# Performance work log

Hardware: AMD Instinct MI355X
Metric: run time of the kernel (lower is better)

The kernel has to match this reference:

```python
import jax, jax.numpy as jnp
import numpy as np

N, E, D = 50000, 640000, 128

def setup_inputs() -> dict:
    key = jax.random.key(0)
    ks = jax.random.split(key, 7)
    feat = jax.random.normal(ks[0], (N, D), dtype=jnp.float32)
    node_alpha = jax.random.uniform(ks[1], (N, 1), dtype=jnp.float32)
    edge_src = jax.random.randint(ks[2], (E,), 0, N, dtype=jnp.int32)
    edge_dst = jax.random.randint(ks[3], (E,), 0, N, dtype=jnp.int32)
    edge_e = jax.random.uniform(ks[4], (E,), dtype=jnp.float32)
    # xavier_normal with relu gain for a square D x D linear
    gain = float(np.sqrt(2.0))
    std = gain * float(np.sqrt(2.0 / (D + D)))
    W = jax.random.normal(ks[5], (D, D), dtype=jnp.float32) * std
    b = jnp.zeros((D,), dtype=jnp.float32)
    return {"feat": feat, "node_alpha": node_alpha, "edge_src": edge_src,
            "edge_dst": edge_dst, "edge_e": edge_e, "W": W, "b": b}

def reference(feat, node_alpha, edge_src, edge_dst, edge_e, W, b):
    # dropout prob = 0 -> identity
    feat_dst = node_alpha[:, 0:1] * feat  # residual term, n_dst == N
    # per-edge: e * Linear(z_src)   (Linear: z @ W.T + b)
    z_src = feat[edge_src]                              # [E, D] gather
    msg = edge_e[:, None] * (z_src @ W.T + b)           # [E, D]
    # mean over each dst node's mailbox
    summed = jax.ops.segment_sum(msg, edge_dst, num_segments=N)          # [N, D]
    deg = jax.ops.segment_sum(jnp.ones((E,), jnp.float32), edge_dst, num_segments=N)
    mean = summed / jnp.maximum(deg, 1.0)[:, None]
    f = jax.nn.relu(mean)
    return f + feat_dst
```

## Files before the change

kernel.cpp:

```cpp
#include <hip/hip_runtime.h>

#define D 128
#define CAP 48
#define NB 196
#define BCAP 3712
#define SPB 5
#define POISON_INT ((int)0xAAAAAAAA)


typedef __attribute__((ext_vector_type(8))) short short8;
typedef __attribute__((ext_vector_type(4))) float f32x4;

__device__ __forceinline__ float bf16bits_to_f(unsigned int u16) {
    return __uint_as_float(u16 << 16);
}
__device__ __forceinline__ unsigned int f_to_bf16bits(float f) {
    return (__float_as_uint(f) + 0x8000u) >> 16;
}
__device__ __forceinline__ void bf16_split(float x, unsigned int& hb, unsigned int& lb) {
    unsigned int u = __float_as_uint(x);
    hb = (u + 0x8000u) >> 16;
    float r = x - __uint_as_float(hb << 16);
    lb = (__float_as_uint(r) + 0x8000u) >> 16;
}

__global__ __launch_bounds__(512) void combo_k(
    const float* __restrict__ feat,
    const float* __restrict__ W,
    const float* __restrict__ b,
    const int* __restrict__ esrc,
    const int* __restrict__ edst,
    const float* __restrict__ ee,
    int* __restrict__ bktcur,
    uint2* __restrict__ bkt,
    unsigned short* __restrict__ h,
    int N, int E, int GB, int n_strips)
{
    __shared__ unsigned int Ab[2][16 * 128];
    __shared__ int hist[256];
    __shared__ int hbase[256];

    const int tid = threadIdx.x;

    if ((int)blockIdx.x >= GB) {
        const int e0 = ((int)blockIdx.x - GB) * 2048 + tid;
        for (int i = tid; i < 256; i += 512) hist[i] = 0;
        __syncthreads();

        int dd[4]; unsigned int pk[4]; int ofs[4]; bool vv[4];
#pragma unroll
        for (int k = 0; k < 4; ++k) {
            int idx = e0 + k * 512;
            vv[k] = idx < E;
            int s = vv[k] ? idx : 0;
            dd[k] = edst[s];
            pk[k] = (f_to_bf16bits(ee[s]) << 16) | ((unsigned int)esrc[s] & 0xFFFFu);
            ofs[k] = vv[k] ? atomicAdd(&hist[dd[k] >> 8], 1) : 0;
        }
        __syncthreads();
        for (int i = tid; i < NB; i += 512) {
            int c = hist[i];
            hbase[i] = c ? (atomicAdd(&bktcur[i], c) - POISON_INT) : 0;
        }
        __syncthreads();
#pragma unroll
        for (int k = 0; k < 4; ++k) {
            if (vv[k]) {
                int bn = dd[k] >> 8;
                int pos = hbase[bn] + ofs[k];
                if (pos < BCAP)
                    bkt[(size_t)bn * BCAP + pos] =
                        make_uint2(pk[k], (unsigned int)(dd[k] & 255));
            }
        }
        return;
    }

    const int w  = tid >> 6;
    const int l  = tid & 63;
    const int lr = l & 15;
    const int cg = l >> 4;

    const int col = w * 16 + lr;
    short8 bh[4], bl[4];
    {
        const float* wrow = W + (size_t)col * D + cg * 8;
#pragma unroll
        for (int kc = 0; kc < 4; ++kc) {
            float4 w0 = *(const float4*)&wrow[kc * 32];
            float4 w1 = *(const float4*)&wrow[kc * 32 + 4];
            unsigned int hb[8], lb[8];
            bf16_split(w0.x, hb[0], lb[0]); bf16_split(w0.y, hb[1], lb[1]);
            bf16_split(w0.z, hb[2], lb[2]); bf16_split(w0.w, hb[3], lb[3]);
            bf16_split(w1.x, hb[4], lb[4]); bf16_split(w1.y, hb[5], lb[5]);
            bf16_split(w1.z, hb[6], lb[6]); bf16_split(w1.w, hb[7], lb[7]);
            union { unsigned int u[4]; short8 s; } uh, ul;
#pragma unroll
            for (int t2 = 0; t2 < 4; ++t2) {
                uh.u[t2] = hb[2 * t2] | (hb[2 * t2 + 1] << 16);
                ul.u[t2] = lb[2 * t2] | (lb[2 * t2 + 1] << 16);
            }
            bh[kc] = uh.s; bl[kc] = ul.s;
        }
    }
    const float bcol = b[col];

    const int sr  = tid >> 5;
    const int sc  = tid & 31;
    const int scs = sc ^ (sr & 7);

    const int strip0 = (int)blockIdx.x * SPB;

    {
        int row = strip0 * 16 + sr;
        float4 a = make_float4(0.f, 0.f, 0.f, 0.f);
        if (row < N) a = *(const float4*)&feat[(size_t)row * D + sc * 4];
        unsigned int hb2, lb2; uint4 pv;
        bf16_split(a.x, hb2, lb2); pv.x = (hb2 << 16) | lb2;
        bf16_split(a.y, hb2, lb2); pv.y = (hb2 << 16) | lb2;
        bf16_split(a.z, hb2, lb2); pv.z = (hb2 << 16) | lb2;
        bf16_split(a.w, hb2, lb2); pv.w = (hb2 << 16) | lb2;
        *(uint4*)&Ab[0][sr * 128 + scs * 4] = pv;
    }
    __syncthreads();

    for (int s = 0; s < SPB; ++s) {
        int sg = strip0 + s;
        if (sg >= n_strips) break;

        float4 anext = make_float4(0.f, 0.f, 0.f, 0.f);
        bool more = (s + 1 < SPB) && (sg + 1 < n_strips);
        if (more) {
            int row = (sg + 1) * 16 + sr;
            if (row < N) anext = *(const float4*)&feat[(size_t)row * D + sc * 4];
        }

        const unsigned int* Ar = &Ab[s & 1][0];
        f32x4 ahh = {0.f, 0.f, 0.f, 0.f};
        f32x4 ahl = {0.f, 0.f, 0.f, 0.f};
        f32x4 alh = {0.f, 0.f, 0.f, 0.f};
#pragma unroll
        for (int kc = 0; kc < 4; ++kc) {
            int ch0 = kc * 8 + cg * 2;
            uint4 ua = *(const uint4*)&Ar[lr * 128 + (((ch0    ) ^ (lr & 7)) << 2)];
            uint4 ub = *(const uint4*)&Ar[lr * 128 + (((ch0 + 1) ^ (lr & 7)) << 2)];
            union { unsigned int u[4]; short8 s; } ah, al;
            ah.u[0] = (ua.x >> 16) | (ua.y & 0xFFFF0000u);
            ah.u[1] = (ua.z >> 16) | (ua.w & 0xFFFF0000u);
            ah.u[2] = (ub.x >> 16) | (ub.y & 0xFFFF0000u);
            ah.u[3] = (ub.z >> 16) | (ub.w & 0xFFFF0000u);
            al.u[0] = (ua.x & 0xFFFFu) | (ua.y << 16);
            al.u[1] = (ua.z & 0xFFFFu) | (ua.w << 16);
            al.u[2] = (ub.x & 0xFFFFu) | (ub.y << 16);
            al.u[3] = (ub.z & 0xFFFFu) | (ub.w << 16);
            ahh = __builtin_amdgcn_mfma_f32_16x16x32_bf16(ah.s, bh[kc], ahh, 0, 0, 0);
            ahl = __builtin_amdgcn_mfma_f32_16x16x32_bf16(ah.s, bl[kc], ahl, 0, 0, 0);
            alh = __builtin_amdgcn_mfma_f32_16x16x32_bf16(al.s, bh[kc], alh, 0, 0, 0);
        }

        {
            int rbase = sg * 16 + cg * 4;
#pragma unroll
            for (int q = 0; q < 4; ++q) {
                int row = rbase + q;
                if (row < N) {
                    float v = ahh[q] + ahl[q] + alh[q] + bcol;
                    h[(size_t)row * D + col] = (unsigned short)f_to_bf16bits(v);
                }
            }
        }

        if (more) {
            unsigned int hb2, lb2; uint4 pv;
            bf16_split(anext.x, hb2, lb2); pv.x = (hb2 << 16) | lb2;
            bf16_split(anext.y, hb2, lb2); pv.y = (hb2 << 16) | lb2;
            bf16_split(anext.z, hb2, lb2); pv.z = (hb2 << 16) | lb2;
            bf16_split(anext.w, hb2, lb2); pv.w = (hb2 << 16) | lb2;
            *(uint4*)&Ab[(s + 1) & 1][sr * 128 + scs * 4] = pv;
        }
        __syncthreads();
    }
}

#define ACC_EDGE(e_, hv_) do { \
    a0 += (e_) * bf16bits_to_f((hv_).x & 0xFFFFu); \
    a1 += (e_) * bf16bits_to_f((hv_).x >> 16); \
    a2 += (e_) * bf16bits_to_f((hv_).y & 0xFFFFu); \
    a3 += (e_) * bf16bits_to_f((hv_).y >> 16); \
} while (0)

__global__ __launch_bounds__(512) void agg_bin_k(
    const float* __restrict__ feat,
    const unsigned short* __restrict__ h,
    const uint2* __restrict__ bkt,
    const int* __restrict__ bktcur,
    const float* __restrict__ alpha,
    float* __restrict__ out,
    int N)
{
    __shared__ int cnt[32];
    __shared__ __align__(16) unsigned int list[32 * CAP];

    const int tid  = threadIdx.x;
    const int bin  = (int)blockIdx.x >> 3;
    const int oct  = (int)blockIdx.x & 7;
    const int node0 = bin * 256 + oct * 32;

    if (tid < 32) cnt[tid] = 0;
    __syncthreads();

    int m = bktcur[bin] - POISON_INT;
    if (m > BCAP) m = BCAP;
    const uint2* B = bkt + (size_t)bin * BCAP;

    uint2 ebuf[8]; bool ev[8];
#pragma unroll
    for (int r = 0; r < 8; ++r) {
        int idx = tid + r * 512;
        ev[r] = idx < m;
        ebuf[r] = B[ev[r] ? idx : 0];
    }
#pragma unroll
    for (int r = 0; r < 8; ++r) {
        int ld = ev[r] ? ((int)ebuf[r].y - oct * 32) : -1;
        if (ld >= 0 && ld < 32) {
            int s = atomicAdd(&cnt[ld], 1);
            if (s < CAP) list[ld * CAP + s] = ebuf[r].x;
        }
    }
    __syncthreads();

    const int l32 = tid & 31;
    const int nl0 = (tid >> 5) * 2;

    for (int nl = nl0; nl < nl0 + 2; ++nl) {
        int node = node0 + nl;
        if (node >= N) break;
        int deg = cnt[nl];
        int c = deg > CAP ? CAP : deg;
        const unsigned int* L = &list[nl * CAP];

        float a0 = 0.f, a1 = 0.f, a2 = 0.f, a3 = 0.f;
        int j = 0;
        for (; j + 8 <= c; j += 8) {
            uint4 qa = *(const uint4*)&L[j];
            uint4 qb = *(const uint4*)&L[j + 4];
            uint2 hv0 = ((const uint2*)(h + (size_t)(qa.x & 0xFFFFu) * D))[l32];
            uint2 hv1 = ((const uint2*)(h + (size_t)(qa.y & 0xFFFFu) * D))[l32];
            uint2 hv2 = ((const uint2*)(h + (size_t)(qa.z & 0xFFFFu) * D))[l32];
            uint2 hv3 = ((const uint2*)(h + (size_t)(qa.w & 0xFFFFu) * D))[l32];
            uint2 hv4 = ((const uint2*)(h + (size_t)(qb.x & 0xFFFFu) * D))[l32];
            uint2 hv5 = ((const uint2*)(h + (size_t)(qb.y & 0xFFFFu) * D))[l32];
            uint2 hv6 = ((const uint2*)(h + (size_t)(qb.z & 0xFFFFu) * D))[l32];
            uint2 hv7 = ((const uint2*)(h + (size_t)(qb.w & 0xFFFFu) * D))[l32];
            ACC_EDGE(bf16bits_to_f(qa.x >> 16), hv0);
            ACC_EDGE(bf16bits_to_f(qa.y >> 16), hv1);
            ACC_EDGE(bf16bits_to_f(qa.z >> 16), hv2);
            ACC_EDGE(bf16bits_to_f(qa.w >> 16), hv3);
            ACC_EDGE(bf16bits_to_f(qb.x >> 16), hv4);
            ACC_EDGE(bf16bits_to_f(qb.y >> 16), hv5);
            ACC_EDGE(bf16bits_to_f(qb.z >> 16), hv6);
            ACC_EDGE(bf16bits_to_f(qb.w >> 16), hv7);
        }
        for (; j + 4 <= c; j += 4) {
            uint4 q = *(const uint4*)&L[j];
            uint2 hv0 = ((const uint2*)(h + (size_t)(q.x & 0xFFFFu) * D))[l32];
            uint2 hv1 = ((const uint2*)(h + (size_t)(q.y & 0xFFFFu) * D))[l32];
            uint2 hv2 = ((const uint2*)(h + (size_t)(q.z & 0xFFFFu) * D))[l32];
            uint2 hv3 = ((const uint2*)(h + (size_t)(q.w & 0xFFFFu) * D))[l32];
            ACC_EDGE(bf16bits_to_f(q.x >> 16), hv0);
            ACC_EDGE(bf16bits_to_f(q.y >> 16), hv1);
            ACC_EDGE(bf16bits_to_f(q.z >> 16), hv2);
            ACC_EDGE(bf16bits_to_f(q.w >> 16), hv3);
        }
        for (; j < c; ++j) {
            unsigned int q = L[j];
            uint2 hv = ((const uint2*)(h + (size_t)(q & 0xFFFFu) * D))[l32];
            ACC_EDGE(bf16bits_to_f(q >> 16), hv);
        }

        float inv = 1.0f / fmaxf((float)deg, 1.0f);
        float al = alpha[node];
        float4 f = ((const float4*)(feat + (size_t)node * D))[l32];
        float4 o;
        o.x = fmaxf(a0 * inv, 0.0f) + al * f.x;
        o.y = fmaxf(a1 * inv, 0.0f) + al * f.y;
        o.z = fmaxf(a2 * inv, 0.0f) + al * f.z;
        o.w = fmaxf(a3 * inv, 0.0f) + al * f.w;
        ((float4*)(out + (size_t)node * D))[l32] = o;
    }
}

extern "C" void kernel_launch(void* const* d_in, const int* in_sizes, int n_in,
                              void* d_out, int out_size, void* d_ws, size_t ws_size,
                              hipStream_t stream) {
    const float* feat  = (const float*)d_in[0];
    const float* alpha = (const float*)d_in[1];
    const int*   esrc  = (const int*)d_in[2];
    const int*   edst  = (const int*)d_in[3];
    const float* ee    = (const float*)d_in[4];
    const float* W     = (const float*)d_in[5];
    const float* b     = (const float*)d_in[6];
    float* out = (float*)d_out;

    const int E = in_sizes[2];
    const int N = in_sizes[0] / D;

    uint2*          bkt    = (uint2*)d_ws;
    int*            bktcur = (int*)(bkt + (size_t)NB * BCAP);
    unsigned short* h      = (unsigned short*)(bktcur + 256);

    const int n_strips = (N + 15) / 16;
    const int GB = (n_strips + SPB - 1) / SPB;
    const int FA = (E + 2047) / 2048;

    combo_k<<<GB + FA, 512, 0, stream>>>(feat, W, b, esrc, edst, ee,
                                         bktcur, bkt, h, N, E, GB, n_strips);

    agg_bin_k<<<NB * 8, 512, 0, stream>>>(feat, h, bkt, bktcur, alpha, out, N);
}
```

Baseline: 136.3 us.

## Process 64 nodes per aggregation block and prefetch residual features

Each aggregation block now handles 64 destination nodes instead of 32, so every bin's edge bucket is read and filtered by 4 blocks rather than 8. That halves the redundant bucket scanning. Each warp now processes 4 nodes, and the residual feat and alpha loads for all four are issued before the gather loops so their latency overlaps the gathers. In exchange the grid has half as many blocks (784), LDS use doubles, and per-thread register pressure rises, which could reduce parallelism and occupancy.

```diff
diff --git a/kernel.cpp b/kernel.cpp
--- a/kernel.cpp
+++ b/kernel.cpp
@@ -198,15 +198,15 @@
     float* __restrict__ out,
     int N)
 {
-    __shared__ int cnt[32];
-    __shared__ __align__(16) unsigned int list[32 * CAP];
+    __shared__ int cnt[64];
+    __shared__ __align__(16) unsigned int list[64 * CAP];
 
     const int tid  = threadIdx.x;
-    const int bin  = (int)blockIdx.x >> 3;
-    const int oct  = (int)blockIdx.x & 7;
-    const int node0 = bin * 256 + oct * 32;
-
-    if (tid < 32) cnt[tid] = 0;
+    const int bin  = (int)blockIdx.x >> 2;
+    const int quar = (int)blockIdx.x & 3;
+    const int node0 = bin * 256 + quar * 64;
+
+    if (tid < 64) cnt[tid] = 0;
     __syncthreads();
 
     int m = bktcur[bin] - POISON_INT;
@@ -222,8 +222,8 @@
     }
 #pragma unroll
     for (int r = 0; r < 8; ++r) {
-        int ld = ev[r] ? ((int)ebuf[r].y - oct * 32) : -1;
-        if (ld >= 0 && ld < 32) {
+        int ld = ev[r] ? ((int)ebuf[r].y - quar * 64) : -1;
+        if (ld >= 0 && ld < 64) {
             int s = atomicAdd(&cnt[ld], 1);
             if (s < CAP) list[ld * CAP + s] = ebuf[r].x;
         }
@@ -231,12 +231,25 @@
     __syncthreads();
 
     const int l32 = tid & 31;
-    const int nl0 = (tid >> 5) * 2;
-
-    for (int nl = nl0; nl < nl0 + 2; ++nl) {
+    const int nl0 = (tid >> 5) * 4;
+
+    float4 fv[4]; float av[4]; int degv[4];
+#pragma unroll
+    for (int t = 0; t < 4; ++t) {
+        int node = node0 + nl0 + t;
+        bool ok = node < N;
+        fv[t] = ok ? ((const float4*)(feat + (size_t)node * D))[l32]
+                   : make_float4(0.f, 0.f, 0.f, 0.f);
+        av[t] = ok ? alpha[node] : 0.f;
+        degv[t] = cnt[nl0 + t];
+    }
+
+#pragma unroll
+    for (int t = 0; t < 4; ++t) {
+        int nl = nl0 + t;
         int node = node0 + nl;
         if (node >= N) break;
-        int deg = cnt[nl];
+        int deg = degv[t];
         int c = deg > CAP ? CAP : deg;
         const unsigned int* L = &list[nl * CAP];
 
@@ -280,13 +293,11 @@
         }
 
         float inv = 1.0f / fmaxf((float)deg, 1.0f);
-        float al = alpha[node];
-        float4 f = ((const float4*)(feat + (size_t)node * D))[l32];
         float4 o;
-        o.x = fmaxf(a0 * inv, 0.0f) + al * f.x;
-        o.y = fmaxf(a1 * inv, 0.0f) + al * f.y;
-        o.z = fmaxf(a2 * inv, 0.0f) + al * f.z;
-        o.w = fmaxf(a3 * inv, 0.0f) + al * f.w;
+        o.x = fmaxf(a0 * inv, 0.0f) + av[t] * fv[t].x;
+        o.y = fmaxf(a1 * inv, 0.0f) + av[t] * fv[t].y;
+        o.z = fmaxf(a2 * inv, 0.0f) + av[t] * fv[t].z;
+        o.w = fmaxf(a3 * inv, 0.0f) + av[t] * fv[t].w;
         ((float4*)(out + (size_t)node * D))[l32] = o;
     }
 }
@@ -317,5 +328,5 @@
     combo_k<<<GB + FA, 512, 0, stream>>>(feat, W, b, esrc, edst, ee,
                                          bktcur, bkt, h, N, E, GB, n_strips);
 
-    agg_bin_k<<<NB * 8, 512, 0, stream>>>(feat, h, bkt, bktcur, alpha, out, N);
-}
+    agg_bin_k<<<NB * 4, 512, 0, stream>>>(feat, h, bkt, bktcur, alpha, out, N);
+}
```

Measured after the change: 137.9 us. Within noise of the previous version (+1.2%).
